# Optimization experiments

Hardware: AMD Instinct MI355X
Metric: run time of the kernel (lower is better)

Reference implementation:

```python
import jax, jax.numpy as jnp
import numpy as np

OUT_H = OUT_W = 7
SCALE = 0.25
SR = 2  # sampling_ratio


def setup_inputs() -> dict:
    key = jax.random.key(0)
    k1, k2, k3, k4, k5, k6 = jax.random.split(key, 6)
    B, C, H, W = 2, 256, 200, 304
    N = 1000
    inputs = jax.random.normal(k1, (B, C, H, W), dtype=jnp.float32)
    # rois: (batch_idx, cx, cy, w, h, angle_deg) in IMAGE coords (scale back by 1/SCALE)
    bidx = jax.random.randint(k2, (N,), 0, B).astype(jnp.float32)
    cx = jax.random.uniform(k3, (N,), minval=0.0, maxval=W / SCALE)
    cy = jax.random.uniform(k4, (N,), minval=0.0, maxval=H / SCALE)
    wh = jax.random.uniform(k5, (N, 2), minval=16.0, maxval=256.0)
    ang = jax.random.uniform(k6, (N,), minval=-90.0, maxval=90.0)
    rois = jnp.concatenate([bidx[:, None], cx[:, None], cy[:, None], wh, ang[:, None]], axis=1)
    return {"inputs": inputs, "rois": rois}


def _roi_align_rotated(feats, rois):
    B, C, H, W = feats.shape
    N = rois.shape[0]
    offset = 0.5  # aligned=True continuous-coordinate convention
    bidx = rois[:, 0].astype(jnp.int32)
    cw = rois[:, 1] * SCALE - offset
    ch = rois[:, 2] * SCALE - offset
    rw = rois[:, 3] * SCALE
    rh = rois[:, 4] * SCALE
    theta = rois[:, 5] * (jnp.pi / 180.0)
    cos_t, sin_t = jnp.cos(theta), jnp.sin(theta)

    bin_h = rh / OUT_H
    bin_w = rw / OUT_W
    # fused (bin, subsample) coordinate: t[j] = ph + (iy+0.5)/SR for j = ph*SR+iy
    t_y = (jnp.arange(OUT_H * SR, dtype=feats.dtype) + 0.5) / SR  # [GH]
    t_x = (jnp.arange(OUT_W * SR, dtype=feats.dtype) + 0.5) / SR  # [GW]
    yy = -rh[:, None] / 2.0 + t_y[None, :] * bin_h[:, None]  # [N,GH] roi-local
    xx = -rw[:, None] / 2.0 + t_x[None, :] * bin_w[:, None]  # [N,GW]

    # rotate into feature-map coords
    y = yy[:, :, None] * cos_t[:, None, None] - xx[:, None, :] * sin_t[:, None, None] + ch[:, None, None]
    x = yy[:, :, None] * sin_t[:, None, None] + xx[:, None, :] * cos_t[:, None, None] + cw[:, None, None]

    empty = (y < -1.0) | (y > H) | (x < -1.0) | (x > W)
    y = jnp.clip(y, 0.0, None)
    x = jnp.clip(x, 0.0, None)
    y_low = jnp.clip(jnp.floor(y).astype(jnp.int32), 0, H - 1)
    x_low = jnp.clip(jnp.floor(x).astype(jnp.int32), 0, W - 1)
    y_high = jnp.minimum(y_low + 1, H - 1)
    x_high = jnp.minimum(x_low + 1, W - 1)
    ly = jnp.clip(y - y_low.astype(y.dtype), 0.0, 1.0)
    lx = jnp.clip(x - x_low.astype(x.dtype), 0.0, 1.0)
    hy, hx = 1.0 - ly, 1.0 - lx

    b = bidx[:, None, None]  # [N,1,1] broadcasts with [N,GH,GW] index arrays
    v1 = feats[b, :, y_low, x_low]    # [N,GH,GW,C]
    v2 = feats[b, :, y_low, x_high]
    v3 = feats[b, :, y_high, x_low]
    v4 = feats[b, :, y_high, x_high]

    w1 = (hy * hx)[..., None]
    w2 = (hy * lx)[..., None]
    w3 = (ly * hx)[..., None]
    w4 = (ly * lx)[..., None]
    val = w1 * v1 + w2 * v2 + w3 * v3 + w4 * v4  # [N,GH,GW,C]
    val = jnp.where(empty[..., None], 0.0, val)

    # average the SRxSR samples within each output bin
    val = val.reshape(rois.shape[0], OUT_H, SR, OUT_W, SR, C).mean(axis=(2, 4))
    return jnp.transpose(val, (0, 3, 1, 2))  # [N,C,OUT_H,OUT_W]


def reference(inputs, rois):
    return _roi_align_rotated(inputs, rois)
```

## Files before the change

### kernel.cpp

```cpp
#include <hip/hip_runtime.h>
#include <math.h>

constexpr int Bn = 2, Cn = 256, Hn = 200, Wn = 304, Nroi = 1000;
constexpr int OH = 7, OW = 7, SRn = 2;
constexpr int NS = OH * SRn;
constexpr int NP = NS * NS;
constexpr int NBIN = OH * OW;
constexpr int HWn = Hn * Wn;
constexpr float SCALE = 0.25f;

__device__ __forceinline__ void compute_desc(const float* __restrict__ r, int p,
                                             int& idx, int& dx, int& dyW,
                                             float4& w) {
  float cw = r[1] * SCALE - 0.5f;
  float ch = r[2] * SCALE - 0.5f;
  float rw = r[3] * SCALE;
  float rh = r[4] * SCALE;
  float theta = r[5] * 0.017453292519943295f;
  float cs = cosf(theta), sn = sinf(theta);
  float bin_h = rh * (1.0f / OH);
  float bin_w = rw * (1.0f / OW);
  int ki = p / NS;
  int kj = p - ki * NS;
  float ty = ((float)ki + 0.5f) * (1.0f / SRn);
  float tx = ((float)kj + 0.5f) * (1.0f / SRn);
  float yy = -0.5f * rh + ty * bin_h;
  float xx = -0.5f * rw + tx * bin_w;
  float y = yy * cs - xx * sn + ch;
  float x = yy * sn + xx * cs + cw;
  bool empty = (y < -1.0f) || (y > (float)Hn) || (x < -1.0f) || (x > (float)Wn);
  y = fmaxf(y, 0.0f);
  x = fmaxf(x, 0.0f);
  int yl = min(max((int)floorf(y), 0), Hn - 1);
  int xl = min(max((int)floorf(x), 0), Wn - 1);
  int yh = min(yl + 1, Hn - 1);
  int xh = min(xl + 1, Wn - 1);
  float ly = fminf(fmaxf(y - (float)yl, 0.0f), 1.0f);
  float lx = fminf(fmaxf(x - (float)xl, 0.0f), 1.0f);
  float hy = 1.0f - ly, hx = 1.0f - lx;
  if (empty) {
    w.x = w.y = w.z = w.w = 0.0f;
  } else {
    w.x = hy * hx;
    w.y = hy * lx;
    w.z = ly * hx;
    w.w = ly * lx;
  }
  idx = yl * Wn + xl;
  dx = xh - xl;
  dyW = (yh - yl) * Wn;
}

__device__ __forceinline__ unsigned bf16rne(float f) {
  unsigned u = __float_as_uint(f);
  return (u + 0x7fffu + ((u >> 16) & 1u)) >> 16;
}
__device__ __forceinline__ unsigned bf16pack(float lo, float hi) {
  return bf16rne(lo) | (bf16rne(hi) << 16);
}

constexpr int TPX = 64, TCH = 64, LP = TPX + 1;
__global__ __launch_bounds__(256) void transpose_bf16(const float* __restrict__ feats,
                                                      unsigned short* __restrict__ ft) {
  __shared__ float tile[TCH * LP];
  int p0 = blockIdx.x * TPX;
  int c0 = blockIdx.y * TCH;
  int b = blockIdx.z;
  int t = threadIdx.x;
  int px4 = t & 15, ch = t >> 4;
#pragma unroll
  for (int i = 0; i < 4; ++i) {
    int c = ch + 16 * i;
    const float4 v = *(const float4*)(feats + ((size_t)b * Cn + c0 + c) * HWn + p0 + px4 * 4);
    tile[c * LP + px4 * 4 + 0] = v.x;
    tile[c * LP + px4 * 4 + 1] = v.y;
    tile[c * LP + px4 * 4 + 2] = v.z;
    tile[c * LP + px4 * 4 + 3] = v.w;
  }
  __syncthreads();
  int o = t & 7;
  int px8 = t >> 3;
#pragma unroll
  for (int pass = 0; pass < 2; ++pass) {
    int p = px8 + 32 * pass;
    uint4 w4;
    w4.x = bf16pack(tile[(o * 8 + 0) * LP + p], tile[(o * 8 + 1) * LP + p]);
    w4.y = bf16pack(tile[(o * 8 + 2) * LP + p], tile[(o * 8 + 3) * LP + p]);
    w4.z = bf16pack(tile[(o * 8 + 4) * LP + p], tile[(o * 8 + 5) * LP + p]);
    w4.w = bf16pack(tile[(o * 8 + 6) * LP + p], tile[(o * 8 + 7) * LP + p]);
    *(uint4*)((char*)ft + (((size_t)b * HWn + p0 + p) * Cn + c0 + o * 8) * 2) = w4;
  }
}

__global__ __launch_bounds__(256, 2) void roi_gather6(const unsigned short* __restrict__ ft,
                                                      const float* __restrict__ rois,
                                                      float* __restrict__ out) {
  __shared__ int4 s_m[NP];
  __shared__ float4 s_w[NP];
  __shared__ __align__(16) float s_out[64 * NBIN];
  int n = blockIdx.x;
  int cg = blockIdx.y;
  const float* r = rois + (size_t)n * 6;
  int t = threadIdx.x;
  if (t < NP) {
    int idx, dx, dy;
    float4 w;
    compute_desc(r, t, idx, dx, dy, w);
    s_m[t] = make_int4(idx * (Cn * 2), dx * (Cn * 2), dy * (Cn * 2), 0);
    s_w[t] = w;
  }
  __syncthreads();
  int b = (int)r[0];
  int lane = t & 63;
  int wv = t >> 6;
  int o = lane & 7;
  int g = lane >> 3;
  const char* fb = (const char*)ft + ((size_t)b * HWn * Cn + cg * 64 + o * 8) * 2;

#pragma unroll
  for (int it = 0; it < 2; ++it) {
    int bin = it * 32 + wv * 8 + g;
    if (bin < NBIN) {
      int bi = bin / OW;
      int bj = bin - bi * OW;
      int p00 = (bi * 2) * NS + bj * 2;
      float acc0 = 0.f, acc1 = 0.f, acc2 = 0.f, acc3 = 0.f;
      float acc4 = 0.f, acc5 = 0.f, acc6 = 0.f, acc7 = 0.f;
#pragma unroll
      for (int s = 0; s < 4; ++s) {
        int p = p00 + (s >> 1) * NS + (s & 1);
        int4 m = s_m[p];
        float4 w = s_w[p];
        const char* A = fb + m.x;
        uint4 v1 = *(const uint4*)(A);
        uint4 v2 = *(const uint4*)(A + m.y);
        uint4 v3 = *(const uint4*)(A + m.z);
        uint4 v4 = *(const uint4*)(A + m.z + m.y);
#define ACC(vv, ww)                                                        \
        acc0 += (ww) * __uint_as_float((vv).x << 16);                      \
        acc1 += (ww) * __uint_as_float((vv).x & 0xffff0000u);              \
        acc2 += (ww) * __uint_as_float((vv).y << 16);                      \
        acc3 += (ww) * __uint_as_float((vv).y & 0xffff0000u);              \
        acc4 += (ww) * __uint_as_float((vv).z << 16);                      \
        acc5 += (ww) * __uint_as_float((vv).z & 0xffff0000u);              \
        acc6 += (ww) * __uint_as_float((vv).w << 16);                      \
        acc7 += (ww) * __uint_as_float((vv).w & 0xffff0000u);
        ACC(v1, w.x)
        ACC(v2, w.y)
        ACC(v3, w.z)
        ACC(v4, w.w)
#undef ACC
      }
      s_out[(o * 8 + 0) * NBIN + bin] = acc0 * 0.25f;
      s_out[(o * 8 + 1) * NBIN + bin] = acc1 * 0.25f;
      s_out[(o * 8 + 2) * NBIN + bin] = acc2 * 0.25f;
      s_out[(o * 8 + 3) * NBIN + bin] = acc3 * 0.25f;
      s_out[(o * 8 + 4) * NBIN + bin] = acc4 * 0.25f;
      s_out[(o * 8 + 5) * NBIN + bin] = acc5 * 0.25f;
      s_out[(o * 8 + 6) * NBIN + bin] = acc6 * 0.25f;
      s_out[(o * 8 + 7) * NBIN + bin] = acc7 * 0.25f;
    }
  }
  __syncthreads();
  const float4* s4 = (const float4*)s_out;
  float4* o4 = (float4*)(out + (size_t)n * Cn * NBIN + (size_t)cg * 64 * NBIN);
#pragma unroll
  for (int k = 0; k < 3; ++k) {
    o4[t + 256 * k] = s4[t + 256 * k];
  }
  if (t < 784 - 3 * 256) {
    o4[t + 256 * 3] = s4[t + 256 * 3];
  }
}

__global__ __launch_bounds__(256) void roi_direct(const float* __restrict__ feats,
                                                  const float* __restrict__ rois,
                                                  float* __restrict__ out) {
  __shared__ int s_idx[NP];
  __shared__ int s_dx[NP];
  __shared__ int s_dy[NP];
  __shared__ float4 s_w[NP];
  int n = blockIdx.x;
  const float* r = rois + (size_t)n * 6;
  int t = threadIdx.x;
  if (t < NP) {
    int idx, dx, dy;
    float4 w;
    compute_desc(r, t, idx, dx, dy, w);
    s_idx[t] = idx;
    s_dx[t] = dx;
    s_dy[t] = dy;
    s_w[t] = w;
  }
  __syncthreads();
  int b = (int)r[0];
  const float* f = feats + ((size_t)b * Cn + t) * HWn;
  float* o = out + ((size_t)n * Cn + t) * NBIN;
  for (int bi = 0; bi < OH; ++bi) {
    for (int bj = 0; bj < OW; ++bj) {
      float acc = 0.0f;
#pragma unroll
      for (int s = 0; s < 4; ++s) {
        int p = (bi * 2 + (s >> 1)) * NS + bj * 2 + (s & 1);
        int idx = s_idx[p];
        int dx = s_dx[p];
        int dy = s_dy[p];
        float4 w = s_w[p];
        acc += w.x * f[idx] + w.y * f[idx + dx] + w.z * f[idx + dy] + w.w * f[idx + dy + dx];
      }
      o[bi * OW + bj] = acc * 0.25f;
    }
  }
}

extern "C" void kernel_launch(void* const* d_in, const int* in_sizes, int n_in,
                              void* d_out, int out_size, void* d_ws, size_t ws_size,
                              hipStream_t stream) {
  const float* feats = (const float*)d_in[0];
  const float* rois = (const float*)d_in[1];
  float* out = (float*)d_out;

  size_t need = (size_t)Bn * HWn * Cn * sizeof(unsigned short);
  if (ws_size >= need) {
    unsigned short* ft = (unsigned short*)d_ws;
    transpose_bf16<<<dim3(HWn / TPX, Cn / TCH, Bn), 256, 0, stream>>>(feats, ft);
    roi_gather6<<<dim3(Nroi, Cn / 64), 256, 0, stream>>>(ft, rois, out);
  } else {
    roi_direct<<<Nroi, 256, 0, stream>>>(feats, rois, out);
  }
}
```

Measured before the change: 241.9 us.

## Process all channels per ROI block, splitting bilinear corners across half-waves

The gather kernel now uses one block per ROI covering all 256 channels, instead of four channel-group blocks that each recomputed the sampling descriptors. Within a wave, 32 lanes each cover 8 channels and the two half-waves each load one x-column pair of corners; the halves are combined with a cross-lane xor shuffle. Bins are processed in two phases through a smaller shared staging buffer, so occupancy can be raised to 4 blocks per SM. In exchange the output writes become strided scalar stores instead of float4 stores, there are extra barriers, and the grid has a quarter as many blocks.

New measurement: 278.2 us. 1.15x slower.

```diff
diff --git a/kernel.cpp b/kernel.cpp
--- a/kernel.cpp
+++ b/kernel.cpp
@@ -92,14 +92,14 @@
   }
 }
 
-__global__ __launch_bounds__(256, 2) void roi_gather6(const unsigned short* __restrict__ ft,
+constexpr int HB1 = 25;
+__global__ __launch_bounds__(256, 4) void roi_gather7(const unsigned short* __restrict__ ft,
                                                       const float* __restrict__ rois,
                                                       float* __restrict__ out) {
   __shared__ int4 s_m[NP];
   __shared__ float4 s_w[NP];
-  __shared__ __align__(16) float s_out[64 * NBIN];
+  __shared__ __align__(16) float s_out[Cn * HB1];
   int n = blockIdx.x;
-  int cg = blockIdx.y;
   const float* r = rois + (size_t)n * 6;
   int t = threadIdx.x;
   if (t < NP) {
@@ -113,14 +113,16 @@
   int b = (int)r[0];
   int lane = t & 63;
   int wv = t >> 6;
-  int o = lane & 7;
-  int g = lane >> 3;
-  const char* fb = (const char*)ft + ((size_t)b * HWn * Cn + cg * 64 + o * 8) * 2;
-
-#pragma unroll
-  for (int it = 0; it < 2; ++it) {
-    int bin = it * 32 + wv * 8 + g;
-    if (bin < NBIN) {
+  int k = lane & 31;
+  int q = lane >> 5;
+  const char* fb = (const char*)ft + (size_t)b * HWn * Cn * 2 + (size_t)k * 16;
+  float* ob = out + (size_t)n * Cn * NBIN;
+
+#pragma unroll 1
+  for (int ph = 0; ph < 2; ++ph) {
+    int b0 = ph ? HB1 : 0;
+    int b1 = ph ? NBIN : HB1;
+    for (int bin = b0 + wv; bin < b1; bin += 4) {
       int bi = bin / OW;
       int bj = bin - bi * OW;
       int p00 = (bi * 2) * NS + bj * 2;
@@ -131,11 +133,11 @@
         int p = p00 + (s >> 1) * NS + (s & 1);
         int4 m = s_m[p];
         float4 w = s_w[p];
-        const char* A = fb + m.x;
-        uint4 v1 = *(const uint4*)(A);
-        uint4 v2 = *(const uint4*)(A + m.y);
-        uint4 v3 = *(const uint4*)(A + m.z);
-        uint4 v4 = *(const uint4*)(A + m.z + m.y);
+        const char* A = fb + m.x + q * m.y;
+        uint4 vlo = *(const uint4*)(A);
+        uint4 vhi = *(const uint4*)(A + m.z);
+        float wlo = q ? w.y : w.x;
+        float whi = q ? w.w : w.z;
 #define ACC(vv, ww)                                                        \
         acc0 += (ww) * __uint_as_float((vv).x << 16);                      \
         acc1 += (ww) * __uint_as_float((vv).x & 0xffff0000u);              \
@@ -145,31 +147,49 @@
         acc5 += (ww) * __uint_as_float((vv).z & 0xffff0000u);              \
         acc6 += (ww) * __uint_as_float((vv).w << 16);                      \
         acc7 += (ww) * __uint_as_float((vv).w & 0xffff0000u);
-        ACC(v1, w.x)
-        ACC(v2, w.y)
-        ACC(v3, w.z)
-        ACC(v4, w.w)
+        ACC(vlo, wlo)
+        ACC(vhi, whi)
 #undef ACC
       }
-      s_out[(o * 8 + 0) * NBIN + bin] = acc0 * 0.25f;
-      s_out[(o * 8 + 1) * NBIN + bin] = acc1 * 0.25f;
-      s_out[(o * 8 + 2) * NBIN + bin] = acc2 * 0.25f;
-      s_out[(o * 8 + 3) * NBIN + bin] = acc3 * 0.25f;
-      s_out[(o * 8 + 4) * NBIN + bin] = acc4 * 0.25f;
-      s_out[(o * 8 + 5) * NBIN + bin] = acc5 * 0.25f;
-      s_out[(o * 8 + 6) * NBIN + bin] = acc6 * 0.25f;
-      s_out[(o * 8 + 7) * NBIN + bin] = acc7 * 0.25f;
+      acc0 += __shfl_xor(acc0, 32);
+      acc1 += __shfl_xor(acc1, 32);
+      acc2 += __shfl_xor(acc2, 32);
+      acc3 += __shfl_xor(acc3, 32);
+      acc4 += __shfl_xor(acc4, 32);
+      acc5 += __shfl_xor(acc5, 32);
+      acc6 += __shfl_xor(acc6, 32);
+      acc7 += __shfl_xor(acc7, 32);
+      if (q == 0) {
+        int col = bin - b0;
+        s_out[(k * 8 + 0) * HB1 + col] = acc0 * 0.25f;
+        s_out[(k * 8 + 1) * HB1 + col] = acc1 * 0.25f;
+        s_out[(k * 8 + 2) * HB1 + col] = acc2 * 0.25f;
+        s_out[(k * 8 + 3) * HB1 + col] = acc3 * 0.25f;
+        s_out[(k * 8 + 4) * HB1 + col] = acc4 * 0.25f;
+        s_out[(k * 8 + 5) * HB1 + col] = acc5 * 0.25f;
+        s_out[(k * 8 + 6) * HB1 + col] = acc6 * 0.25f;
+        s_out[(k * 8 + 7) * HB1 + col] = acc7 * 0.25f;
+      }
     }
-  }
-  __syncthreads();
-  const float4* s4 = (const float4*)s_out;
-  float4* o4 = (float4*)(out + (size_t)n * Cn * NBIN + (size_t)cg * 64 * NBIN);
-#pragma unroll
-  for (int k = 0; k < 3; ++k) {
-    o4[t + 256 * k] = s4[t + 256 * k];
-  }
-  if (t < 784 - 3 * 256) {
-    o4[t + 256 * 3] = s4[t + 256 * 3];
+    __syncthreads();
+    if (ph == 0) {
+#pragma unroll
+      for (int i2 = 0; i2 < 25; ++i2) {
+        int idx = t + 256 * i2;
+        int c = idx / 25;
+        int bn = idx - c * 25;
+        ob[c * NBIN + bn] = s_out[idx];
+      }
+    } else {
+#pragma unroll
+      for (int i2 = 0; i2 < 24; ++i2) {
+        int idx = t + 256 * i2;
+        int c = idx / 24;
+        int bn = idx - c * 24;
+        ob[c * NBIN + HB1 + bn] = s_out[c * HB1 + bn];
+      }
+    }
+    __syncthreads();
   }
 }
 
@@ -224,7 +244,7 @@
   if (ws_size >= need) {
     unsigned short* ft = (unsigned short*)d_ws;
     transpose_bf16<<<dim3(HWn / TPX, Cn / TCH, Bn), 256, 0, stream>>>(feats, ft);
-    roi_gather6<<<dim3(Nroi, Cn / 64), 256, 0, stream>>>(ft, rois, out);
+    roi_gather7<<<dim3(Nroi), 256, 0, stream>>>(ft, rois, out);
   } else {
     roi_direct<<<Nroi, 256, 0, stream>>>(feats, rois, out);
   }
```
